# Optimization experiments

Measured on AMD Instinct MI355X. Metric: run time of the kernel, lower is better.

The kernel has to match this reference:

```python
import jax, jax.numpy as jnp
import numpy as np

B, N, H, D_OUT, T = 32, 2048, 256, 64, 12

def setup_inputs() -> dict:
    key = jax.random.key(0)
    ks = jax.random.split(key, 7)
    s = lambda fan_in: 1.0 / np.sqrt(fan_in)
    return {
        "x": T,  # horizon (python int)
        "h": jax.random.normal(ks[0], (B, N, H), dtype=jnp.float32),
        "gate_w": jax.random.uniform(ks[1], (2 * H, 2 * H), jnp.float32, -s(2 * H), s(2 * H)),
        "gate_b": jax.random.uniform(ks[2], (2 * H,), jnp.float32, -s(2 * H), s(2 * H)),
        "out_w": jax.random.uniform(ks[3], (H, 2 * H), jnp.float32, -s(2 * H), s(2 * H)),
        "out_b": jax.random.uniform(ks[4], (H,), jnp.float32, -s(2 * H), s(2 * H)),
        "proj_w": jax.random.uniform(ks[5], (D_OUT, H), jnp.float32, -s(H), s(H)),
        "proj_b": jax.random.uniform(ks[6], (D_OUT,), jnp.float32, -s(H), s(H)),
    }


def reference(x, h, gate_w, gate_b, out_w, out_b, proj_w, proj_b):
    # add_extern_factor=False, num_layer=1: at each step, cell input == current
    # hidden state (state = h[-1]; h[0] is the same tensor).
    shape = h.shape
    hf = h.reshape(-1, shape[-1])  # (b, H), b = B*N

    def step(hc, _):
        xh = jnp.concatenate([hc, hc], axis=-1)          # (b, 2H): input==h
        gates = xh @ gate_w.T + gate_b                   # (b, 2H)
        r, z = jnp.split(gates, 2, axis=-1)
        r = jax.nn.sigmoid(r)
        z = jax.nn.sigmoid(z)
        xh2 = jnp.concatenate([hc, r * hc], axis=-1)     # (b, 2H)
        h_new = jnp.tanh(xh2 @ out_w.T + out_b)          # (b, H)
        hn = z * hc + (1.0 - z) * h_new
        out = hn @ proj_w.T + proj_b                     # (b, D_OUT)
        return hn, out

    _, outs = jax.lax.scan(step, hf, None, length=x)     # (T, b, D_OUT)
    outs = jnp.moveaxis(outs, 0, 1)                      # (b, T, D_OUT)
    out = outs.reshape(shape[:-1] + (x, outs.shape[-1])) # (B, N, T, D_OUT)
    # transpose(-2, dim=-2) is identity
    return out
```

## Files before the change

kernel.cpp:

```cpp
#include <hip/hip_runtime.h>
#include <stdint.h>


#define TSTEPS 12
#define AS3 __attribute__((address_space(3)))

typedef _Float16 f16x8 __attribute__((ext_vector_type(8)));
typedef _Float16 f16x2 __attribute__((ext_vector_type(2)));
typedef float    f32x16 __attribute__((ext_vector_type(16)));
typedef float    f32x4  __attribute__((ext_vector_type(4)));
typedef uint32_t u32x4  __attribute__((ext_vector_type(4)));
typedef uint32_t u32x2  __attribute__((ext_vector_type(2)));

typedef AS3 uint8_t       u8l;
typedef const AS3 uint8_t cu8l;

#define WG_E (512*256)
#define W1_E (256*256)
#define WS_W_F16 (WG_E + 2*W1_E + 64*256)
#define BIAS_F32 832
#define WS_BYTES (WS_W_F16*2 + BIAS_F32*4)

__global__ void prep_weights(const float* __restrict__ gw,
                             const float* __restrict__ ow,
                             const float* __restrict__ pw,
                             const float* __restrict__ gb,
                             const float* __restrict__ ob,
                             const float* __restrict__ pb,
                             _Float16* __restrict__ ws)
{
    int idx = blockIdx.x*256 + threadIdx.x;
    if (idx < WG_E) {
        int j = idx >> 8, k = idx & 255;
        ws[idx] = (_Float16)(gw[j*512 + k] + gw[j*512 + 256 + k]);
    } else if (idx < WG_E + W1_E) {
        int i = idx - WG_E; int r = i >> 8, c = i & 255;
        ws[idx] = (_Float16)ow[r*512 + c];
    } else if (idx < WG_E + 2*W1_E) {
        int i = idx - WG_E - W1_E; int r = i >> 8, c = i & 255;
        ws[idx] = (_Float16)ow[r*512 + 256 + c];
    } else if (idx < WS_W_F16) {
        ws[idx] = (_Float16)pw[idx - WG_E - 2*W1_E];
    } else if (idx < WS_W_F16 + BIAS_F32) {
        int b = idx - WS_W_F16;
        float* bd = (float*)(ws + WS_W_F16);
        if (b < 768) {
            int type = b >> 8, r = b & 255;
            int c = r >> 6, n = (r >> 5) & 1, kg = (r >> 4) & 1, e = r & 15;
            int col = 64*c + 32*n + 4*kg + (e & 3) + 8*(e >> 2);
            bd[b] = (type == 0) ? gb[col] : (type == 1) ? gb[256 + col] : ob[col];
        } else {
            int i = b - 768;
            int n = (i >> 5) & 1, kg = (i >> 4) & 1, e = i & 15;
            bd[b] = pb[32*n + 4*kg + (e & 3) + 8*(e >> 2)];
        }
    }
}

__device__ __forceinline__ float sigm(float x) {
    return __builtin_amdgcn_rcpf(1.0f + __expf(-x));
}
__device__ __forceinline__ float tanh_(float x) {
    return 1.0f - 2.0f*__builtin_amdgcn_rcpf(1.0f + __expf(2.0f*x));
}

__device__ __forceinline__ void stage(const uint8_t* __restrict__ Wp,
                                      u8l* slot, int w, int laneC)
{
    #pragma unroll
    for (int i = 0; i < 4; ++i) {
        int c    = w*4 + i;
        int ks   = c >> 1, tile = c & 1;
        int s    = laneC + tile*16384 + ks*32;
        __builtin_amdgcn_global_load_lds(
            (const __attribute__((address_space(1))) uint32_t*)(Wp + s),
            (AS3 uint32_t*)(slot + w*4096 + i*1024), 16, 0, 0);
    }
}

__device__ __forceinline__ f32x16 ldbias(cu8l* p) {
    f32x16 r;
    #pragma unroll
    for (int j = 0; j < 4; ++j) {
        f32x4 t = *(const AS3 f32x4*)(p + j*16);
        r[j*4+0]=t[0]; r[j*4+1]=t[1]; r[j*4+2]=t[2]; r[j*4+3]=t[3];
    }
    return r;
}

__device__ __forceinline__ f16x8 pk8(uint32_t w01, uint32_t w23,
                                     uint32_t w45, uint32_t w67) {
    u32x2 p0 = __builtin_amdgcn_permlane32_swap(w01, w45, false, false);
    u32x2 p1 = __builtin_amdgcn_permlane32_swap(w23, w67, false, false);
    u32x4 u = { p0[0], p1[0], p0[1], p1[1] };
    return __builtin_bit_cast(f16x8, u);
}
__device__ __forceinline__ f16x8 pkS(const f32x16& a, int off) {
    f16x2 a01 = {(_Float16)sigm(a[off+0]), (_Float16)sigm(a[off+1])};
    f16x2 a23 = {(_Float16)sigm(a[off+2]), (_Float16)sigm(a[off+3])};
    f16x2 a45 = {(_Float16)sigm(a[off+4]), (_Float16)sigm(a[off+5])};
    f16x2 a67 = {(_Float16)sigm(a[off+6]), (_Float16)sigm(a[off+7])};
    return pk8(__builtin_bit_cast(uint32_t, a01), __builtin_bit_cast(uint32_t, a23),
               __builtin_bit_cast(uint32_t, a45), __builtin_bit_cast(uint32_t, a67));
}
__device__ __forceinline__ f16x8 pkT(const f32x16& a, int off) {
    f16x2 a01 = {(_Float16)tanh_(a[off+0]), (_Float16)tanh_(a[off+1])};
    f16x2 a23 = {(_Float16)tanh_(a[off+2]), (_Float16)tanh_(a[off+3])};
    f16x2 a45 = {(_Float16)tanh_(a[off+4]), (_Float16)tanh_(a[off+5])};
    f16x2 a67 = {(_Float16)tanh_(a[off+6]), (_Float16)tanh_(a[off+7])};
    return pk8(__builtin_bit_cast(uint32_t, a01), __builtin_bit_cast(uint32_t, a23),
               __builtin_bit_cast(uint32_t, a45), __builtin_bit_cast(uint32_t, a67));
}

__device__ __forceinline__ void gemm2(cu8l* panL, const f16x8* B,
                                      f32x16& a0, f32x16& a1) {
    #pragma unroll
    for (int ks = 0; ks < 16; ++ks) {
        f16x8 w0 = *(const AS3 f16x8*)(panL + ks*2048);
        f16x8 w1 = *(const AS3 f16x8*)(panL + ks*2048 + 1024);
        a0 = __builtin_amdgcn_mfma_f32_32x32x16_f16(w0, B[ks], a0, 0, 0, 0);
        a1 = __builtin_amdgcn_mfma_f32_32x32x16_f16(w1, B[ks], a1, 0, 0, 0);
    }
}

#define PHASE(SP, ...) do {                                                 \
    asm volatile("s_waitcnt vmcnt(4)" ::: "memory");                        \
    asm volatile("s_waitcnt lgkmcnt(0)" ::: "memory");                      \
    __builtin_amdgcn_s_barrier();                                           \
    asm volatile("" ::: "memory");                                          \
    stage(W + (SP)*32768, WbL + sS*32768, w, laneC);                        \
    { cu8l* panL = WbL + sC*32768 + LB; __VA_ARGS__; }                      \
    sC = (sC == 2) ? 0 : sC + 1;                                            \
    sS = (sS == 2) ? 0 : sS + 1;                                            \
} while (0)

__global__ __launch_bounds__(512, 1)
void gru_dec(const float* __restrict__ h_in, const _Float16* __restrict__ Wf,
             float* __restrict__ out)
{
    __shared__ __align__(16) uint8_t lds_[101632];
    u8l* ldsb = (u8l*)lds_;
    u8l* WbL  = ldsb;
    u8l* biasL = ldsb + 98304;
    const uint8_t* W = (const uint8_t*)Wf;

    const int tid  = threadIdx.x;
    const int lane = tid & 63;
    const int w    = tid >> 6;
    const int bl31 = lane & 31;
    const int kg   = lane >> 5;
    const size_t rowg = (size_t)blockIdx.x*256 + w*32 + bl31;

    const int laneC = bl31*512 + kg*16;
    const int LB    = lane*16;

    f16x8 h[16], rh[16], hn[16];
    {
        const float* hs = h_in + rowg*256 + kg*8;
        #pragma unroll
        for (int ks = 0; ks < 16; ++ks) {
            f32x4 x = *(const f32x4*)(hs + ks*16);
            f32x4 y = *(const f32x4*)(hs + ks*16 + 4);
            f16x8 v = {(_Float16)x[0],(_Float16)x[1],(_Float16)x[2],(_Float16)x[3],
                       (_Float16)y[0],(_Float16)y[1],(_Float16)y[2],(_Float16)y[3]};
            h[ks] = v;
        }
    }
    {
        const float* bsrc = (const float*)(Wf + WS_W_F16);
        for (int i = tid; i < BIAS_F32; i += 512)
            *(AS3 float*)(biasL + i*4) = bsrc[i];
    }
    __syncthreads();

    cu8l* bK = biasL + kg*64;

    stage(W + 0*32768, WbL,         w, laneC);
    stage(W + 1*32768, WbL + 32768, w, laneC);
    int sC = 0, sS = 2;

    for (int t = 0; t < TSTEPS; ++t) {
        f32x16 o0, o1;
        f16x8 zb[4];

#define RPH(SP_STG, C)                                                        \
        PHASE(SP_STG, {                                                       \
            f32x16 a0 = ldbias(bK + (C)*256);                                 \
            f32x16 a1 = ldbias(bK + (C)*256 + 128);                           \
            gemm2(panL, h, a0, a1);                                           \
            rh[4*(C)+0] = pkS(a0, 0)*h[4*(C)+0];                              \
            rh[4*(C)+1] = pkS(a0, 8)*h[4*(C)+1];                              \
            rh[4*(C)+2] = pkS(a1, 0)*h[4*(C)+2];                              \
            rh[4*(C)+3] = pkS(a1, 8)*h[4*(C)+3]; })
        RPH(2, 0); RPH(3, 1); RPH(4, 2); RPH(8, 3);
#undef RPH

#define ZPH(SP_STG, C)                                                        \
        PHASE(SP_STG, {                                                       \
            f32x16 a0 = ldbias(bK + 1024 + (C)*256);                          \
            f32x16 a1 = ldbias(bK + 1024 + (C)*256 + 128);                    \
            gemm2(panL, h, a0, a1);                                           \
            zb[0] = pkS(a0, 0); zb[1] = pkS(a0, 8);                           \
            zb[2] = pkS(a1, 0); zb[3] = pkS(a1, 8); })
#define W1PH(SP_STG, C)                                                       \
        PHASE(SP_STG, {                                                       \
            o0 = ldbias(bK + 2048 + (C)*256);                                 \
            o1 = ldbias(bK + 2048 + (C)*256 + 128);                           \
            gemm2(panL, h, o0, o1); })
#define W2PH(SP_STG, C)                                                       \
        PHASE(SP_STG, {                                                       \
            gemm2(panL, rh, o0, o1);                                          \
            f16x8 u0 = pkT(o0, 0), u1 = pkT(o0, 8);                           \
            f16x8 u2 = pkT(o1, 0), u3 = pkT(o1, 8);                           \
            hn[4*(C)+0] = u0 + zb[0]*(h[4*(C)+0] - u0);                       \
            hn[4*(C)+1] = u1 + zb[1]*(h[4*(C)+1] - u1);                       \
            hn[4*(C)+2] = u2 + zb[2]*(h[4*(C)+2] - u2);                       \
            hn[4*(C)+3] = u3 + zb[3]*(h[4*(C)+3] - u3); })

        ZPH(12, 0); W1PH(5, 0); W2PH(9,  0);
        ZPH(13, 1); W1PH(6, 1); W2PH(10, 1);
        ZPH(14, 2); W1PH(7, 2); W2PH(11, 2);
        ZPH(15, 3); W1PH(16,3); W2PH(0,  3);
#undef ZPH
#undef W1PH
#undef W2PH

        #pragma unroll
        for (int i = 0; i < 16; ++i) h[i] = hn[i];

        PHASE(1, {
            f32x16 a0 = ldbias(bK + 3072);
            f32x16 a1 = ldbias(bK + 3072 + 128);
            gemm2(panL, h, a0, a1);
            float* op = out + (rowg*TSTEPS + t)*64 + 4*kg;
            _Pragma("unroll")
            for (int j = 0; j < 4; ++j) {
                f32x4 v0 = {a0[4*j], a0[4*j+1], a0[4*j+2], a0[4*j+3]};
                f32x4 v1 = {a1[4*j], a1[4*j+1], a1[4*j+2], a1[4*j+3]};
                *(f32x4*)(op + 8*j)      = v0;
                *(f32x4*)(op + 32 + 8*j) = v1;
            }
        });
    }
}

extern "C" void kernel_launch(void* const* d_in, const int* in_sizes, int n_in,
                              void* d_out, int out_size, void* d_ws, size_t ws_size,
                              hipStream_t stream) {
    const float* h  = (const float*)d_in[1];
    const float* gw = (const float*)d_in[2];
    const float* gb = (const float*)d_in[3];
    const float* ow = (const float*)d_in[4];
    const float* ob = (const float*)d_in[5];
    const float* pw = (const float*)d_in[6];
    const float* pb = (const float*)d_in[7];
    if (ws_size < (size_t)WS_BYTES) return;
    _Float16* ws = (_Float16*)d_ws;

    hipLaunchKernelGGL(prep_weights, dim3((WS_W_F16 + BIAS_F32 + 255)/256), dim3(256),
                       0, stream, gw, ow, pw, gb, ob, pb, ws);
    hipLaunchKernelGGL(gru_dec, dim3(65536/256), dim3(512), 0, stream,
                       h, ws, (float*)d_out);
}
```

Before: 574.1 us.

## Fold biases into weight panels as an extra K column via MFMA

Each weight matrix row is padded with an extra column holding the bias (stored in fp16), and an extra MFMA against a constant 'ones' B-vector adds the bias. This removes the fp32 bias LDS loads and accumulator initialisation from every phase. In exchange each staged panel grows by 25% (five 1KB chunks per wave instead of four), adding global-to-LDS traffic, LDS footprint and an extra pair of MFMAs per gemm. Biases also lose precision by being rounded to fp16.

```diff
diff --git a/kernel.cpp b/kernel.cpp
--- a/kernel.cpp
+++ b/kernel.cpp
@@ -15,11 +15,12 @@
 typedef AS3 uint8_t       u8l;
 typedef const AS3 uint8_t cu8l;
 
-#define WG_E (512*256)
-#define W1_E (256*256)
-#define WS_W_F16 (WG_E + 2*W1_E + 64*256)
-#define BIAS_F32 832
-#define WS_BYTES (WS_W_F16*2 + BIAS_F32*4)
+#define NROWS_W   1088
+#define KCOLS     272
+#define ROWB      (KCOLS*2)
+#define PANB      (64*ROWB)
+#define WS_TOTAL_F16 (NROWS_W*KCOLS)
+#define WS_BYTES  (WS_TOTAL_F16*2)
 
 __global__ void prep_weights(const float* __restrict__ gw,
                              const float* __restrict__ ow,
@@ -30,31 +31,25 @@
                              _Float16* __restrict__ ws)
 {
     int idx = blockIdx.x*256 + threadIdx.x;
-    if (idx < WG_E) {
-        int j = idx >> 8, k = idx & 255;
-        ws[idx] = (_Float16)(gw[j*512 + k] + gw[j*512 + 256 + k]);
-    } else if (idx < WG_E + W1_E) {
-        int i = idx - WG_E; int r = i >> 8, c = i & 255;
-        ws[idx] = (_Float16)ow[r*512 + c];
-    } else if (idx < WG_E + 2*W1_E) {
-        int i = idx - WG_E - W1_E; int r = i >> 8, c = i & 255;
-        ws[idx] = (_Float16)ow[r*512 + 256 + c];
-    } else if (idx < WS_W_F16) {
-        ws[idx] = (_Float16)pw[idx - WG_E - 2*W1_E];
-    } else if (idx < WS_W_F16 + BIAS_F32) {
-        int b = idx - WS_W_F16;
-        float* bd = (float*)(ws + WS_W_F16);
-        if (b < 768) {
-            int type = b >> 8, r = b & 255;
-            int c = r >> 6, n = (r >> 5) & 1, kg = (r >> 4) & 1, e = r & 15;
-            int col = 64*c + 32*n + 4*kg + (e & 3) + 8*(e >> 2);
-            bd[b] = (type == 0) ? gb[col] : (type == 1) ? gb[256 + col] : ob[col];
-        } else {
-            int i = b - 768;
-            int n = (i >> 5) & 1, kg = (i >> 4) & 1, e = i & 15;
-            bd[b] = pb[32*n + 4*kg + (e & 3) + 8*(e >> 2)];
-        }
-    }
+    if (idx >= WS_TOTAL_F16) return;
+    int row = idx / KCOLS, col = idx - row*KCOLS;
+    float v = 0.0f;
+    if (row < 512) {
+        if (col < 256)      v = gw[row*512 + col] + gw[row*512 + 256 + col];
+        else if (col == 256) v = gb[row];
+    } else if (row < 768) {
+        int r = row - 512;
+        if (col < 256)      v = ow[r*512 + col];
+        else if (col == 256) v = ob[r];
+    } else if (row < 1024) {
+        int r = row - 768;
+        if (col < 256)      v = ow[r*512 + 256 + col];
+    } else {
+        int r = row - 1024;
+        if (col < 256)      v = pw[r*256 + col];
+        else if (col == 256) v = pb[r];
+    }
+    ws[idx] = (_Float16)v;
 }
 
 __device__ __forceinline__ float sigm(float x) {
@@ -68,24 +63,14 @@
                                       u8l* slot, int w, int laneC)
 {
     #pragma unroll
-    for (int i = 0; i < 4; ++i) {
-        int c    = w*4 + i;
+    for (int i = 0; i < 5; ++i) {
+        int c    = w*5 + i;
         int ks   = c >> 1, tile = c & 1;
-        int s    = laneC + tile*16384 + ks*32;
+        int s    = (c < 34) ? (laneC + tile*(32*ROWB) + ks*32) : laneC;
         __builtin_amdgcn_global_load_lds(
             (const __attribute__((address_space(1))) uint32_t*)(Wp + s),
-            (AS3 uint32_t*)(slot + w*4096 + i*1024), 16, 0, 0);
-    }
-}
-
-__device__ __forceinline__ f32x16 ldbias(cu8l* p) {
-    f32x16 r;
-    #pragma unroll
-    for (int j = 0; j < 4; ++j) {
-        f32x4 t = *(const AS3 f32x4*)(p + j*16);
-        r[j*4+0]=t[0]; r[j*4+1]=t[1]; r[j*4+2]=t[2]; r[j*4+3]=t[3];
-    }
-    return r;
+            (AS3 uint32_t*)(slot + c*1024), 16, 0, 0);
+    }
 }
 
 __device__ __forceinline__ f16x8 pk8(uint32_t w01, uint32_t w23,
@@ -112,8 +97,8 @@
                __builtin_bit_cast(uint32_t, a45), __builtin_bit_cast(uint32_t, a67));
 }
 
-__device__ __forceinline__ void gemm2(cu8l* panL, const f16x8* B,
-                                      f32x16& a0, f32x16& a1) {
+__device__ __forceinline__ void gemm16(cu8l* panL, const f16x8* B,
+                                       f32x16& a0, f32x16& a1) {
     #pragma unroll
     for (int ks = 0; ks < 16; ++ks) {
         f16x8 w0 = *(const AS3 f16x8*)(panL + ks*2048);
@@ -122,14 +107,22 @@
         a1 = __builtin_amdgcn_mfma_f32_32x32x16_f16(w1, B[ks], a1, 0, 0, 0);
     }
 }
+__device__ __forceinline__ void gemm17(cu8l* panL, const f16x8* B, f16x8 hb,
+                                       f32x16& a0, f32x16& a1) {
+    gemm16(panL, B, a0, a1);
+    f16x8 w0 = *(const AS3 f16x8*)(panL + 32*1024);
+    f16x8 w1 = *(const AS3 f16x8*)(panL + 33*1024);
+    a0 = __builtin_amdgcn_mfma_f32_32x32x16_f16(w0, hb, a0, 0, 0, 0);
+    a1 = __builtin_amdgcn_mfma_f32_32x32x16_f16(w1, hb, a1, 0, 0, 0);
+}
 
 #define PHASE(SP, ...) do {                                                 \
-    asm volatile("s_waitcnt vmcnt(4)" ::: "memory");                        \
+    asm volatile("s_waitcnt vmcnt(5)" ::: "memory");                        \
     asm volatile("s_waitcnt lgkmcnt(0)" ::: "memory");                      \
     __builtin_amdgcn_s_barrier();                                           \
     asm volatile("" ::: "memory");                                          \
-    stage(W + (SP)*32768, WbL + sS*32768, w, laneC);                        \
-    { cu8l* panL = WbL + sC*32768 + LB; __VA_ARGS__; }                      \
+    stage(W + (size_t)(SP)*PANB, WbL + sS*40960, w, laneC);                 \
+    { cu8l* panL = WbL + sC*40960 + LB; __VA_ARGS__; }                      \
     sC = (sC == 2) ? 0 : sC + 1;                                            \
     sS = (sS == 2) ? 0 : sS + 1;                                            \
 } while (0)
@@ -138,10 +131,8 @@
 void gru_dec(const float* __restrict__ h_in, const _Float16* __restrict__ Wf,
              float* __restrict__ out)
 {
-    __shared__ __align__(16) uint8_t lds_[101632];
-    u8l* ldsb = (u8l*)lds_;
-    u8l* WbL  = ldsb;
-    u8l* biasL = ldsb + 98304;
+    __shared__ __align__(16) uint8_t lds_[122880];
+    u8l* WbL = (u8l*)lds_;
     const uint8_t* W = (const uint8_t*)Wf;
 
     const int tid  = threadIdx.x;
@@ -151,8 +142,11 @@
     const int kg   = lane >> 5;
     const size_t rowg = (size_t)blockIdx.x*256 + w*32 + bl31;
 
-    const int laneC = bl31*512 + kg*16;
+    const int laneC = bl31*ROWB + kg*16;
     const int LB    = lane*16;
+
+    f16x8 hb = {};
+    if (kg == 0) hb[0] = (_Float16)1.0f;
 
     f16x8 h[16], rh[16], hn[16];
     {
@@ -166,17 +160,10 @@
             h[ks] = v;
         }
     }
-    {
-        const float* bsrc = (const float*)(Wf + WS_W_F16);
-        for (int i = tid; i < BIAS_F32; i += 512)
-            *(AS3 float*)(biasL + i*4) = bsrc[i];
-    }
     __syncthreads();
 
-    cu8l* bK = biasL + kg*64;
-
-    stage(W + 0*32768, WbL,         w, laneC);
-    stage(W + 1*32768, WbL + 32768, w, laneC);
+    stage(W + 0*PANB, WbL,         w, laneC);
+    stage(W + 1*PANB, WbL + 40960, w, laneC);
     int sC = 0, sS = 2;
 
     for (int t = 0; t < TSTEPS; ++t) {
@@ -185,9 +172,8 @@
 
 #define RPH(SP_STG, C)                                                        \
         PHASE(SP_STG, {                                                       \
-            f32x16 a0 = ldbias(bK + (C)*256);                                 \
-            f32x16 a1 = ldbias(bK + (C)*256 + 128);                           \
-            gemm2(panL, h, a0, a1);                                           \
+            f32x16 a0 = {}, a1 = {};                                          \
+            gemm17(panL, h, hb, a0, a1);                                      \
             rh[4*(C)+0] = pkS(a0, 0)*h[4*(C)+0];                              \
             rh[4*(C)+1] = pkS(a0, 8)*h[4*(C)+1];                              \
             rh[4*(C)+2] = pkS(a1, 0)*h[4*(C)+2];                              \
@@ -197,19 +183,17 @@
 
 #define ZPH(SP_STG, C)                                                        \
         PHASE(SP_STG, {                                                       \
-            f32x16 a0 = ldbias(bK + 1024 + (C)*256);                          \
-            f32x16 a1 = ldbias(bK + 1024 + (C)*256 + 128);                    \
-            gemm2(panL, h, a0, a1);                                           \
+            f32x16 a0 = {}, a1 = {};                                          \
+            gemm17(panL, h, hb, a0, a1);                                      \
             zb[0] = pkS(a0, 0); zb[1] = pkS(a0, 8);                           \
             zb[2] = pkS(a1, 0); zb[3] = pkS(a1, 8); })
 #define W1PH(SP_STG, C)                                                       \
         PHASE(SP_STG, {                                                       \
-            o0 = ldbias(bK + 2048 + (C)*256);                                 \
-            o1 = ldbias(bK + 2048 + (C)*256 + 128);                           \
-            gemm2(panL, h, o0, o1); })
+            o0 = (f32x16){}; o1 = (f32x16){};                                 \
+            gemm17(panL, h, hb, o0, o1); })
 #define W2PH(SP_STG, C)                                                       \
         PHASE(SP_STG, {                                                       \
-            gemm2(panL, rh, o0, o1);                                          \
+            gemm16(panL, rh, o0, o1);                                         \
             f16x8 u0 = pkT(o0, 0), u1 = pkT(o0, 8);                           \
             f16x8 u2 = pkT(o1, 0), u3 = pkT(o1, 8);                           \
             hn[4*(C)+0] = u0 + zb[0]*(h[4*(C)+0] - u0);                       \
@@ -229,9 +213,8 @@
         for (int i = 0; i < 16; ++i) h[i] = hn[i];
 
         PHASE(1, {
-            f32x16 a0 = ldbias(bK + 3072);
-            f32x16 a1 = ldbias(bK + 3072 + 128);
-            gemm2(panL, h, a0, a1);
+            f32x16 a0 = {}, a1 = {};
+            gemm17(panL, h, hb, a0, a1);
             float* op = out + (rowg*TSTEPS + t)*64 + 4*kg;
             _Pragma("unroll")
             for (int j = 0; j < 4; ++j) {
@@ -257,7 +240,7 @@
     if (ws_size < (size_t)WS_BYTES) return;
     _Float16* ws = (_Float16*)d_ws;
 
-    hipLaunchKernelGGL(prep_weights, dim3((WS_W_F16 + BIAS_F32 + 255)/256), dim3(256),
+    hipLaunchKernelGGL(prep_weights, dim3((WS_TOTAL_F16 + 255)/256), dim3(256),
                        0, stream, gw, ow, pw, gb, ob, pb, ws);
     hipLaunchKernelGGL(gru_dec, dim3(65536/256), dim3(512), 0, stream,
                        h, ws, (float*)d_out);
```

Result: slower. 665.0 us (+15.8%).
